# Kernel optimization log

Hardware: AMD Instinct MI355X
Metric: run time of the kernel (lower is better)

Reference implementation:

```python
import jax, jax.numpy as jnp
import numpy as np

EPS_NORM = 1e-12  # torch F.normalize eps


def _resize_bilinear_ac(x, H, W):
    # Bilinear resize with align_corners=True on NCHW tensor x.
    h, w = x.shape[-2], x.shape[-1]
    ys = jnp.linspace(0.0, h - 1.0, H)
    xs = jnp.linspace(0.0, w - 1.0, W)
    y0 = jnp.floor(ys).astype(jnp.int32); y1 = jnp.minimum(y0 + 1, h - 1)
    x0 = jnp.floor(xs).astype(jnp.int32); x1 = jnp.minimum(x0 + 1, w - 1)
    wy = (ys - y0).astype(x.dtype)[None, None, :, None]
    wx = (xs - x0).astype(x.dtype)
    rows = x[:, :, y0, :] * (1 - wy) + x[:, :, y1, :] * wy  # (B,C,H,w)
    return rows[:, :, :, x0] * (1 - wx) + rows[:, :, :, x1] * wx  # (B,C,H,W)


def _icc(p, b):
    # p: (b, 19, hw) row-stochastic over hw.
    # M[i, j] = KLDiv(input=p_i, target=p_j, batchmean) = (1/b) * sum p_j*(log p_j - p_i)
    # NOTE: original code passes probabilities (not log-probs) as KLDiv input; kept faithful.
    E = jnp.sum(p * jnp.log(p), axis=(0, 2))            # (19,) sum_b,k p log p
    G = jnp.einsum('bik,bjk->ij', p, p)                  # (19,19) sum_b,k p_i p_j
    M = (E[None, :] - G) / b
    sym = jnp.triu(M) + jnp.triu(M, 1).T                 # loop writes value for i<=j to both [i,j],[j,i]
    nrm = jnp.maximum(jnp.linalg.norm(sym, axis=1, keepdims=True), EPS_NORM)
    return sym / nrm                                     # F.normalize(dim=1)


def reference(s_out, t_out, t_logit, s_logit, conv_w, conv_b):
    T = 1.0  # temperature
    # --- pi_loss ---
    B, C, H, W = t_out.shape
    s1 = _resize_bilinear_ac(s_out, H, W)
    s1 = jnp.einsum('bchw,oc->bohw', s1, conv_w[:, :, 0, 0]) + conv_b[None, :, None, None]
    log_ps = jax.nn.log_softmax(s1 / T, axis=1)
    pt = jax.nn.softmax(t_out / T, axis=1)
    # torch KLDivLoss() default reduction='mean' (mean over ALL elements)
    pi_loss = jnp.mean(pt * (jnp.log(pt) - log_ps))
    # --- lo_loss ---
    b, n, h, w = s_logit.shape
    tl = _resize_bilinear_ac(t_logit, h, w)
    s = jax.nn.softmax(s_logit.reshape(b, n, h * w) / T, axis=2)
    t = jax.nn.softmax(tl.reshape(b, n, h * w) / T, axis=2)
    ICCS = _icc(s, b)
    ICCT = _icc(t, b)
    lo_loss = jnp.sum((ICCS - ICCT) ** 2)
    return pi_loss, lo_loss


def setup_inputs() -> dict:
    key = jax.random.key(0)
    k = jax.random.split(key, 6)
    return {
        's_out': jax.random.normal(k[0], (8, 128, 33, 33), jnp.float32),
        't_out': jax.random.normal(k[1], (8, 768, 65, 65), jnp.float32),
        't_logit': jax.random.normal(k[2], (8, 19, 65, 65), jnp.float32),
        's_logit': jax.random.normal(k[3], (8, 19, 129, 129), jnp.float32),
        'conv_w': jax.random.normal(k[4], (768, 128, 1, 1), jnp.float32) * 0.05,
        'conv_b': jax.random.normal(k[5], (768,), jnp.float32) * 0.05,
    }
```

## Files before the change

### kernel.cpp

```cpp
#include <hip/hip_runtime.h>
#include <math.h>

#define WS_E0   0
#define WS_E1   19
#define WS_G0   64
#define WS_G1   448
#define WS_Z    1152
#define WS_WBF  2048

typedef __bf16 bf16x8 __attribute__((ext_vector_type(8)));
typedef float  f32x4  __attribute__((ext_vector_type(4)));
typedef const __attribute__((address_space(1))) unsigned int guint;
typedef       __attribute__((address_space(3))) unsigned int luint;

__global__ void k_init(const float* __restrict__ conv_w, float* __restrict__ ws,
                       float* __restrict__ out) {
    const int bx = blockIdx.x, tid = threadIdx.x;
    if (bx < 96) {
        __bf16* Wb = (__bf16*)(ws + WS_WBF);
        #pragma unroll
        for (int j = 0; j < 4; j++) {
            int idx = bx * 1024 + j * 256 + tid;
            Wb[idx] = (__bf16)conv_w[idx];
        }
    } else {
        for (int k = tid; k < 2048; k += 256) ws[k] = 0.f;
        if (tid < 2) out[tid] = 0.f;
    }
}

__device__ __forceinline__ float t_resized(const float* __restrict__ Trow, int k) {
    int y = k / 129, x = k - y * 129;
    int y0 = y >> 1, x0 = x >> 1;
    int y1 = y0 + (y & 1), x1 = x0 + (x & 1);
    float fy = 0.5f * (float)(y & 1), fx = 0.5f * (float)(x & 1);
    float v00 = Trow[y0 * 65 + x0], v01 = Trow[y0 * 65 + x1];
    float v10 = Trow[y1 * 65 + x0], v11 = Trow[y1 * 65 + x1];
    float r0 = v00 + fx * (v01 - v00);
    float r1 = v10 + fx * (v11 - v10);
    return r0 + fy * (r1 - r0);
}

__launch_bounds__(256, 3)
__global__ void k_main(const float* __restrict__ s_out, const float* __restrict__ t_out,
                       const float* __restrict__ conv_w, const float* __restrict__ bias,
                       const float* __restrict__ s_logit, const float* __restrict__ t_logit,
                       float* __restrict__ ws, float* __restrict__ out) {
    __shared__ __align__(16) char lds[50176];
    const int tid = threadIdx.x;
    const int bx  = blockIdx.x;

    if (bx >= 304 && bx < 832) {
        const int idx   = bx - 304;
        const int b     = idx / 66;
        const int strip = idx - b * 66;
        const int px0   = strip * 64;

        const int l = tid & 63, g = tid >> 6, q = l >> 4, n = l & 15;
        const int og = g * 16;

        const float* base_t = t_out + (size_t)(b * 768 + og) * 4225;
        int off[4];
        #pragma unroll
        for (int j = 0; j < 4; j++) {
            int col = ((n * 4) + j * 16) & 63;
            off[j] = (j * 4 + q) * 4225 + px0 + col;
        }
        int colr[4];
        #pragma unroll
        for (int pt = 0; pt < 4; pt++)
            colr[pt] = (((pt * 16 + (n & 12) - q * 16) & 63)) + (n & 3);

        auto issue_t = [&](int cc) {
            int k = cc % 3;
            char* lb = (k == 2 ? lds : lds + 17408 + k * 16384) + g * 4096;
            const float* gb = base_t + (size_t)cc * 64 * 4225;
            #pragma unroll
            for (int j = 0; j < 4; j++)
                __builtin_amdgcn_global_load_lds((guint*)(gb + off[j]),
                                                 (luint*)(lb + j * 1024), 16, 0, 0);
        };

        issue_t(0);
        issue_t(1);

        __bf16* xs = (__bf16*)lds;

        {
            const float* Sb = s_out + b * 128 * 1089;
            #pragma unroll
            for (int ii = 0; ii < 32; ii++) {
                int id2 = tid + ii * 256;
                int c = id2 >> 6, px = id2 & 63;
                int hw = px0 + px;
                int h = hw / 65, w = hw - h * 65;
                int y0 = h >> 1, x0 = w >> 1;
                int y1 = y0 + (h & 1), x1 = x0 + (w & 1);
                float wy = 0.5f * (float)(h & 1), wx = 0.5f * (float)(w & 1);
                const float* Sc = Sb + c * 1089;
                float v00 = Sc[y0 * 33 + x0], v01 = Sc[y0 * 33 + x1];
                float v10 = Sc[y1 * 33 + x0], v11 = Sc[y1 * 33 + x1];
                float r0 = v00 + wx * (v01 - v00);
                float r1 = v10 + wx * (v11 - v10);
                xs[px * 136 + c] = (__bf16)(r0 + wy * (r1 - r0));
            }
        }
        asm volatile("s_waitcnt lgkmcnt(0)" ::: "memory");
        __builtin_amdgcn_s_barrier();
        __builtin_amdgcn_sched_barrier(0);

        bf16x8 bfrag[4][4];
        #pragma unroll
        for (int pt = 0; pt < 4; pt++)
            #pragma unroll
            for (int kf = 0; kf < 4; kf++)
                bfrag[pt][kf] = *(const bf16x8*)&xs[(pt * 16 + n) * 136 + kf * 32 + q * 8];

        const __bf16* Wbf = (const __bf16*)(ws + WS_WBF);
        bf16x8 afr[3][4];
        f32x4  bq[3];
        auto load_a = [&](int cc) {
            int s = cc % 3;
            int row0 = cc * 64 + og;
            const __bf16* Wr = Wbf + (size_t)(row0 + n) * 128 + q * 8;
            #pragma unroll
            for (int kf = 0; kf < 4; kf++) afr[s][kf] = *(const bf16x8*)(Wr + kf * 32);
            bq[s] = *(const f32x4*)&bias[row0 + q * 4];
        };
        load_a(0);
        load_a(1);

        asm volatile("s_waitcnt lgkmcnt(0)" ::: "memory");
        __builtin_amdgcn_s_barrier();
        __builtin_amdgcn_sched_barrier(0);
        issue_t(2);

        float Zt[4], St[4], Dd[4], Zs[4];
        #pragma unroll
        for (int pt = 0; pt < 4; pt++) { Zt[pt] = 0.f; St[pt] = 0.f; Dd[pt] = 0.f; Zs[pt] = 0.f; }

        #pragma unroll
        for (int c = 0; c < 12; c++) {
            if (c == 0 || c == 10) asm volatile("s_waitcnt vmcnt(9)"  ::: "memory");
            else if (c == 11)      asm volatile("s_waitcnt vmcnt(0)"  ::: "memory");
            else                   asm volatile("s_waitcnt vmcnt(13)" ::: "memory");

            const int k = c % 3;
            const float* tw = (const float*)((k == 2 ? lds : lds + 17408 + k * 16384) + g * 4096);
            #pragma unroll
            for (int pt = 0; pt < 4; pt++) {
                f32x4 a0 = {0.f, 0.f, 0.f, 0.f};
                #pragma unroll
                for (int kf = 0; kf < 4; kf++)
                    a0 = __builtin_amdgcn_mfma_f32_16x16x32_bf16(afr[k][kf], bfrag[pt][kf], a0, 0, 0, 0);
                #pragma unroll
                for (int r = 0; r < 4; r++) {
                    float tv  = tw[(q * 4 + r) * 64 + colr[pt]];
                    float s1v = a0[r] + bq[k][r];
                    float e   = __expf(tv);
                    Zt[pt] += e;
                    St[pt]  = fmaf(e, tv,  St[pt]);
                    Dd[pt]  = fmaf(e, s1v, Dd[pt]);
                    Zs[pt] += __expf(s1v);
                }
            }
            if (c <= 9) load_a(c + 2);
            if (c <= 8) issue_t(c + 3);
        }

        __syncthreads();
        float* scr = (float*)lds;
        {
            int p = g * 4 + q;
            #pragma unroll
            for (int pt = 0; pt < 4; pt++) {
                f32x4 v = {Zt[pt], St[pt], Dd[pt], Zs[pt]};
                *(f32x4*)&scr[(pt * 16 + n) * 68 + p * 4] = v;
            }
        }
        __syncthreads();
        if (tid < 64) {
            float Z = 0.f, S = 0.f, D = 0.f, Z2 = 0.f;
            #pragma unroll
            for (int p = 0; p < 16; p++) {
                f32x4 v = *(const f32x4*)&scr[tid * 68 + p * 4];
                Z += v[0]; S += v[1]; D += v[2]; Z2 += v[3];
            }
            float contrib = (S - D) / Z - logf(Z) + logf(Z2);
            #pragma unroll
            for (int o = 32; o > 0; o >>= 1) contrib += __shfl_down(contrib, o);
            if (tid == 0) atomicAdd(out, contrib * (1.0f / 25958400.0f));
        }
    } else if (bx < 304) {
        float* red = (float*)lds;
        int row  = bx;
        int side = (row >= 152) ? 1 : 0;
        int r    = side ? row - 152 : row;
        const float* src = side ? (t_logit + r * 4225) : (s_logit + r * 16641);

        float z = 0.f, s = 0.f;
        #pragma unroll 4
        for (int k = tid; k < 16641; k += 256) {
            float v = side ? t_resized(src, k) : src[k];
            float e = __expf(v);
            z += e;
            s = fmaf(e, v, s);
        }
        for (int off = 32; off > 0; off >>= 1) { z += __shfl_down(z, off); s += __shfl_down(s, off); }
        if ((tid & 63) == 0) { red[tid >> 6] = z; red[4 + (tid >> 6)] = s; }
        __syncthreads();
        if (tid == 0) {
            float Z = red[0] + red[1] + red[2] + red[3];
            float S = red[4] + red[5] + red[6] + red[7];
            ws[WS_Z + row] = Z;
            atomicAdd(&ws[(side ? WS_E1 : WS_E0) + (r % 19)], S / Z - logf(Z));
        }
    } else {
        float* xc  = (float*)lds;
        float* red = (float*)lds + 128;
        const int b = bx - 832;
        if (tid < 128) xc[tid] = s_out[((size_t)b * 128 + tid) * 1089 + 1088];
        __syncthreads();
        float z = 0.f, s = 0.f, d = 0.f, z2 = 0.f;
        #pragma unroll
        for (int rep = 0; rep < 3; rep++) {
            int o = tid + rep * 256;
            const float* Wr = conv_w + (size_t)o * 128;
            float s1 = bias[o];
            for (int cc = 0; cc < 128; cc++) s1 = fmaf(Wr[cc], xc[cc], s1);
            float tv = t_out[((size_t)(b * 768 + o)) * 4225 + 4224];
            float e  = __expf(tv);
            z += e; s = fmaf(e, tv, s); d = fmaf(e, s1, d); z2 += __expf(s1);
        }
        for (int off = 32; off > 0; off >>= 1) {
            z += __shfl_down(z, off); s += __shfl_down(s, off);
            d += __shfl_down(d, off); z2 += __shfl_down(z2, off);
        }
        if ((tid & 63) == 0) {
            int wv = tid >> 6;
            red[wv] = z; red[4 + wv] = s; red[8 + wv] = d; red[12 + wv] = z2;
        }
        __syncthreads();
        if (tid == 0) {
            float Z = red[0] + red[1] + red[2] + red[3];
            float S = red[4] + red[5] + red[6] + red[7];
            float D = red[8] + red[9] + red[10] + red[11];
            float Z2 = red[12] + red[13] + red[14] + red[15];
            float contrib = (S - D) / Z - logf(Z) + logf(Z2);
            atomicAdd(out, contrib * (1.0f / 25958400.0f));
        }
    }
}

#define KT 512
#define KP 516
__global__ void k_mid(const float* __restrict__ s_logit, const float* __restrict__ t_logit,
                      float* __restrict__ ws, float* __restrict__ out) {
    __shared__ __align__(16) char lds[39296];
    const int tid = threadIdx.x;
    const int bx  = blockIdx.x;

    float* pbuf  = (float*)lds;
    float* rowiz = (float*)(lds + 39216);
    int side = (bx >= 264) ? 1 : 0;
    int rm   = side ? bx - 264 : bx;
    int b = rm / 33, kt = rm - b * 33;
    int k0 = kt * KT;

    if (tid < 19) rowiz[tid] = 1.0f / ws[WS_Z + side * 152 + b * 19 + tid];
    __syncthreads();

    for (int i = 0; i < 19; i++) {
        const float* src = side ? (t_logit + (size_t)(b * 19 + i) * 4225)
                                : (s_logit + (size_t)(b * 19 + i) * 16641);
        float iz = rowiz[i];
        #pragma unroll
        for (int kl = tid; kl < KT; kl += 256) {
            int k = k0 + kl;
            float p = 0.f;
            if (k < 16641) {
                float v = side ? t_resized(src, k) : src[k];
                p = __expf(v) * iz;
            }
            pbuf[i * KP + kl] = p;
        }
    }
    __syncthreads();

    if (tid < 190) {
        int t = tid, i = 0;
        while (t >= 19 - i) { t -= 19 - i; i++; }
        int j = i + t;
        const float* pi_ = &pbuf[i * KP];
        const float* pj_ = &pbuf[j * KP];
        float g0 = 0.f, g1 = 0.f, g2 = 0.f, g3 = 0.f;
        #pragma unroll 2
        for (int kl = 0; kl < KT; kl += 16) {
            float4 a0 = *(const float4*)&pi_[kl];      float4 c0 = *(const float4*)&pj_[kl];
            float4 a1 = *(const float4*)&pi_[kl + 4];  float4 c1 = *(const float4*)&pj_[kl + 4];
            float4 a2 = *(const float4*)&pi_[kl + 8];  float4 c2 = *(const float4*)&pj_[kl + 8];
            float4 a3 = *(const float4*)&pi_[kl + 12]; float4 c3 = *(const float4*)&pj_[kl + 12];
            g0 = fmaf(a0.x, c0.x, g0); g0 = fmaf(a0.y, c0.y, g0);
            g0 = fmaf(a0.z, c0.z, g0); g0 = fmaf(a0.w, c0.w, g0);
            g1 = fmaf(a1.x, c1.x, g1); g1 = fmaf(a1.y, c1.y, g1);
            g1 = fmaf(a1.z, c1.z, g1); g1 = fmaf(a1.w, c1.w, g1);
            g2 = fmaf(a2.x, c2.x, g2); g2 = fmaf(a2.y, c2.y, g2);
            g2 = fmaf(a2.z, c2.z, g2); g2 = fmaf(a2.w, c2.w, g2);
            g3 = fmaf(a3.x, c3.x, g3); g3 = fmaf(a3.y, c3.y, g3);
            g3 = fmaf(a3.z, c3.z, g3); g3 = fmaf(a3.w, c3.w, g3);
        }
        atomicAdd(&ws[(side ? WS_G1 : WS_G0) + i * 19 + j], (g0 + g1) + (g2 + g3));
    }
}

__global__ void k_final(const float* __restrict__ ws, float* __restrict__ out) {
    __shared__ float Ms[361], Mt[361], ns[19], nt[19];
    __shared__ float red[8];
    int tid = threadIdx.x;
    if (tid < 361) {
        int i = tid / 19, j = tid - i * 19;
        int lo = min(i, j), hi = max(i, j);
        Ms[tid] = (ws[WS_E0 + hi] - ws[WS_G0 + lo * 19 + hi]) * 0.125f;
        Mt[tid] = (ws[WS_E1 + hi] - ws[WS_G1 + lo * 19 + hi]) * 0.125f;
    }
    __syncthreads();
    if (tid < 19) {
        float as = 0.f, at = 0.f;
        for (int j = 0; j < 19; j++) {
            as = fmaf(Ms[tid * 19 + j], Ms[tid * 19 + j], as);
            at = fmaf(Mt[tid * 19 + j], Mt[tid * 19 + j], at);
        }
        ns[tid] = fmaxf(sqrtf(as), 1e-12f);
        nt[tid] = fmaxf(sqrtf(at), 1e-12f);
    }
    __syncthreads();
    float d = 0.f;
    if (tid < 361) {
        int i = tid / 19;
        float v = Ms[tid] / ns[i] - Mt[tid] / nt[i];
        d = v * v;
    }
    for (int off = 32; off > 0; off >>= 1) d += __shfl_down(d, off);
    if ((tid & 63) == 0) red[tid >> 6] = d;
    __syncthreads();
    if (tid == 0) out[1] = red[0] + red[1] + red[2] + red[3] + red[4] + red[5];
}

extern "C" void kernel_launch(void* const* d_in, const int* in_sizes, int n_in,
                              void* d_out, int out_size, void* d_ws, size_t ws_size,
                              hipStream_t stream) {
    const float* s_out   = (const float*)d_in[0];
    const float* t_out   = (const float*)d_in[1];
    const float* t_logit = (const float*)d_in[2];
    const float* s_logit = (const float*)d_in[3];
    const float* conv_w  = (const float*)d_in[4];
    const float* conv_b  = (const float*)d_in[5];
    float* out = (float*)d_out;
    float* ws  = (float*)d_ws;

    k_init<<<dim3(97), dim3(256), 0, stream>>>(conv_w, ws, out);
    k_main<<<dim3(840), dim3(256), 0, stream>>>(s_out, t_out, conv_w, conv_b,
                                                s_logit, t_logit, ws, out);
    k_mid<<<dim3(528), dim3(256), 0, stream>>>(s_logit, t_logit, ws, out);
    k_final<<<dim3(1), dim3(384), 0, stream>>>(ws, out);
}
```

Baseline: 277.3 us.

## Reorder block roles, double-buffer weight fragments, and pin main-loop schedule

Heavy pi-loss GEMM blocks now take the lowest block indices, so they are dispatched before the lighter softmax-row blocks. The weight fragment buffer shrinks from triple to double buffering, which lowers register pressure. The main loop is manually unrolled with sched_barriers and retuned vmcnt waits so loads stay interleaved with MFMA work. The hand-counted vmcnt values depend on the exact number of outstanding loads, so a miscount could produce races or unneeded stalls.

```diff
diff --git a/kernel.cpp b/kernel.cpp
--- a/kernel.cpp
+++ b/kernel.cpp
@@ -50,10 +50,9 @@
     const int tid = threadIdx.x;
     const int bx  = blockIdx.x;
 
-    if (bx >= 304 && bx < 832) {
-        const int idx   = bx - 304;
-        const int b     = idx / 66;
-        const int strip = idx - b * 66;
+    if (bx < 528) {
+        const int b     = bx / 66;
+        const int strip = bx - b * 66;
         const int px0   = strip * 64;
 
         const int l = tid & 63, g = tid >> 6, q = l >> 4, n = l & 15;
@@ -117,10 +116,10 @@
                 bfrag[pt][kf] = *(const bf16x8*)&xs[(pt * 16 + n) * 136 + kf * 32 + q * 8];
 
         const __bf16* Wbf = (const __bf16*)(ws + WS_WBF);
-        bf16x8 afr[3][4];
-        f32x4  bq[3];
+        bf16x8 afr[2][4];
+        f32x4  bq[2];
         auto load_a = [&](int cc) {
-            int s = cc % 3;
+            int s = cc & 1;
             int row0 = cc * 64 + og;
             const __bf16* Wr = Wbf + (size_t)(row0 + n) * 128 + q * 8;
             #pragma unroll
@@ -139,34 +138,50 @@
         #pragma unroll
         for (int pt = 0; pt < 4; pt++) { Zt[pt] = 0.f; St[pt] = 0.f; Dd[pt] = 0.f; Zs[pt] = 0.f; }
 
-        #pragma unroll
-        for (int c = 0; c < 12; c++) {
-            if (c == 0 || c == 10) asm volatile("s_waitcnt vmcnt(9)"  ::: "memory");
-            else if (c == 11)      asm volatile("s_waitcnt vmcnt(0)"  ::: "memory");
-            else                   asm volatile("s_waitcnt vmcnt(13)" ::: "memory");
-
-            const int k = c % 3;
-            const float* tw = (const float*)((k == 2 ? lds : lds + 17408 + k * 16384) + g * 4096);
-            #pragma unroll
-            for (int pt = 0; pt < 4; pt++) {
-                f32x4 a0 = {0.f, 0.f, 0.f, 0.f};
-                #pragma unroll
-                for (int kf = 0; kf < 4; kf++)
-                    a0 = __builtin_amdgcn_mfma_f32_16x16x32_bf16(afr[k][kf], bfrag[pt][kf], a0, 0, 0, 0);
-                #pragma unroll
-                for (int r = 0; r < 4; r++) {
-                    float tv  = tw[(q * 4 + r) * 64 + colr[pt]];
-                    float s1v = a0[r] + bq[k][r];
-                    float e   = __expf(tv);
-                    Zt[pt] += e;
-                    St[pt]  = fmaf(e, tv,  St[pt]);
-                    Dd[pt]  = fmaf(e, s1v, Dd[pt]);
-                    Zs[pt] += __expf(s1v);
-                }
-            }
-            if (c <= 9) load_a(c + 2);
-            if (c <= 8) issue_t(c + 3);
-        }
+#define PI_IT(c, NW)                                                                     \
+        asm volatile("s_waitcnt vmcnt(" #NW ")" ::: "memory");                           \
+        __builtin_amdgcn_sched_barrier(0);                                               \
+        {                                                                                \
+            const float* tw = (const float*)((((c) % 3) == 2 ? lds                       \
+                                : lds + 17408 + ((c) % 3) * 16384) + g * 4096);          \
+            _Pragma("unroll")                                                            \
+            for (int pt = 0; pt < 4; pt++) {                                             \
+                f32x4 a0 = {0.f, 0.f, 0.f, 0.f};                                         \
+                _Pragma("unroll")                                                        \
+                for (int kf = 0; kf < 4; kf++)                                           \
+                    a0 = __builtin_amdgcn_mfma_f32_16x16x32_bf16(afr[(c) & 1][kf],       \
+                                               bfrag[pt][kf], a0, 0, 0, 0);              \
+                _Pragma("unroll")                                                        \
+                for (int r = 0; r < 4; r++) {                                            \
+                    float tv  = tw[(q * 4 + r) * 64 + colr[pt]];                         \
+                    float s1v = a0[r] + bq[(c) & 1][r];                                  \
+                    float e   = __expf(tv);                                              \
+                    Zt[pt] += e;                                                         \
+                    St[pt]  = fmaf(e, tv,  St[pt]);                                      \
+                    Dd[pt]  = fmaf(e, s1v, Dd[pt]);                                      \
+                    Zs[pt] += __expf(s1v);                                               \
+                }                                                                        \
+            }                                                                            \
+        }                                                                                \
+        __builtin_amdgcn_sched_barrier(0);                                               \
+        if ((c) <= 9) load_a((c) + 2);                                                   \
+        __builtin_amdgcn_sched_barrier(0);                                               \
+        if ((c) <= 8) issue_t((c) + 3);                                                  \
+        __builtin_amdgcn_sched_barrier(0);
+
+        PI_IT(0, 18)
+        PI_IT(1, 23)
+        PI_IT(2, 18)
+        PI_IT(3, 18)
+        PI_IT(4, 18)
+        PI_IT(5, 18)
+        PI_IT(6, 18)
+        PI_IT(7, 18)
+        PI_IT(8, 18)
+        PI_IT(9, 18)
+        PI_IT(10, 14)
+        PI_IT(11, 5)
+#undef PI_IT
 
         __syncthreads();
         float* scr = (float*)lds;
@@ -191,9 +206,9 @@
             for (int o = 32; o > 0; o >>= 1) contrib += __shfl_down(contrib, o);
             if (tid == 0) atomicAdd(out, contrib * (1.0f / 25958400.0f));
         }
-    } else if (bx < 304) {
+    } else if (bx < 832) {
         float* red = (float*)lds;
-        int row  = bx;
+        int row  = bx - 528;
         int side = (row >= 152) ? 1 : 0;
         int r    = side ? row - 152 : row;
         const float* src = side ? (t_logit + r * 4225) : (s_logit + r * 16641);
```

New measurement: 262.1 us. 1.06x faster.

## Restructure pi-loss pipeline to double buffering with per-step B-fragment LDS reads

Applied to the files above, without the earlier changes.

Switches the t_out staging from a triple buffer to a double buffer in a separate LDS region, and loads B fragments from LDS on every step instead of holding 16 bf16x8 registers. The xs stride is padded from 136 to 140 to reduce bank conflicts, and the A/bias fragments are ping-ponged through named registers via macros. The main GEMM blocks now come first in block order, ahead of the logit-row blocks, and occupancy is set with waves_per_eu. The goal is to cut register pressure so 3 waves fit, and to start the heavy blocks first. The cost is a shallower prefetch depth and more LDS reads per step.

```diff
diff --git a/kernel.cpp b/kernel.cpp
--- a/kernel.cpp
+++ b/kernel.cpp
@@ -41,19 +41,19 @@
     return r0 + fy * (r1 - r0);
 }
 
-__launch_bounds__(256, 3)
-__global__ void k_main(const float* __restrict__ s_out, const float* __restrict__ t_out,
-                       const float* __restrict__ conv_w, const float* __restrict__ bias,
-                       const float* __restrict__ s_logit, const float* __restrict__ t_logit,
-                       float* __restrict__ ws, float* __restrict__ out) {
-    __shared__ __align__(16) char lds[50176];
+__global__ __launch_bounds__(256)
+__attribute__((amdgpu_waves_per_eu(3, 3)))
+void k_main(const float* __restrict__ s_out, const float* __restrict__ t_out,
+            const float* __restrict__ conv_w, const float* __restrict__ bias,
+            const float* __restrict__ s_logit, const float* __restrict__ t_logit,
+            float* __restrict__ ws, float* __restrict__ out) {
+    __shared__ __align__(16) char lds[50688];
     const int tid = threadIdx.x;
     const int bx  = blockIdx.x;
 
-    if (bx >= 304 && bx < 832) {
-        const int idx   = bx - 304;
-        const int b     = idx / 66;
-        const int strip = idx - b * 66;
+    if (bx < 528) {
+        const int b     = bx / 66;
+        const int strip = bx - b * 66;
         const int px0   = strip * 64;
 
         const int l = tid & 63, g = tid >> 6, q = l >> 4, n = l & 15;
@@ -72,8 +72,7 @@
             colr[pt] = (((pt * 16 + (n & 12) - q * 16) & 63)) + (n & 3);
 
         auto issue_t = [&](int cc) {
-            int k = cc % 3;
-            char* lb = (k == 2 ? lds : lds + 17408 + k * 16384) + g * 4096;
+            char* lb = lds + 17920 + (cc & 1) * 16384 + g * 4096;
             const float* gb = base_t + (size_t)cc * 64 * 4225;
             #pragma unroll
             for (int j = 0; j < 4; j++)
@@ -102,71 +101,75 @@
                 float v10 = Sc[y1 * 33 + x0], v11 = Sc[y1 * 33 + x1];
                 float r0 = v00 + wx * (v01 - v00);
                 float r1 = v10 + wx * (v11 - v10);
-                xs[px * 136 + c] = (__bf16)(r0 + wy * (r1 - r0));
+                xs[px * 140 + c] = (__bf16)(r0 + wy * (r1 - r0));
             }
         }
         asm volatile("s_waitcnt lgkmcnt(0)" ::: "memory");
         __builtin_amdgcn_s_barrier();
         __builtin_amdgcn_sched_barrier(0);
 
-        bf16x8 bfrag[4][4];
-        #pragma unroll
-        for (int pt = 0; pt < 4; pt++)
-            #pragma unroll
-            for (int kf = 0; kf < 4; kf++)
-                bfrag[pt][kf] = *(const bf16x8*)&xs[(pt * 16 + n) * 136 + kf * 32 + q * 8];
-
         const __bf16* Wbf = (const __bf16*)(ws + WS_WBF);
-        bf16x8 afr[3][4];
-        f32x4  bq[3];
-        auto load_a = [&](int cc) {
-            int s = cc % 3;
-            int row0 = cc * 64 + og;
-            const __bf16* Wr = Wbf + (size_t)(row0 + n) * 128 + q * 8;
-            #pragma unroll
-            for (int kf = 0; kf < 4; kf++) afr[s][kf] = *(const bf16x8*)(Wr + kf * 32);
-            bq[s] = *(const f32x4*)&bias[row0 + q * 4];
-        };
-        load_a(0);
-        load_a(1);
-
-        asm volatile("s_waitcnt lgkmcnt(0)" ::: "memory");
-        __builtin_amdgcn_s_barrier();
-        __builtin_amdgcn_sched_barrier(0);
-        issue_t(2);
+        bf16x8 aA0, aA1, aA2, aA3, aB0, aB1, aB2, aB3;
+        f32x4  bqA, bqB;
+
+#define LOAD_A(cc, A0_, A1_, A2_, A3_, BQ_) do {                                          \
+        const __bf16* Wr_ = Wbf + (size_t)((cc) * 64 + og + n) * 128 + q * 8;             \
+        A0_ = *(const bf16x8*)(Wr_);       A1_ = *(const bf16x8*)(Wr_ + 32);              \
+        A2_ = *(const bf16x8*)(Wr_ + 64);  A3_ = *(const bf16x8*)(Wr_ + 96);              \
+        BQ_ = *(const f32x4*)&bias[(cc) * 64 + og + q * 4];                               \
+    } while (0)
+
+        LOAD_A(0, aA0, aA1, aA2, aA3, bqA);
 
         float Zt[4], St[4], Dd[4], Zs[4];
         #pragma unroll
         for (int pt = 0; pt < 4; pt++) { Zt[pt] = 0.f; St[pt] = 0.f; Dd[pt] = 0.f; Zs[pt] = 0.f; }
 
-        #pragma unroll
-        for (int c = 0; c < 12; c++) {
-            if (c == 0 || c == 10) asm volatile("s_waitcnt vmcnt(9)"  ::: "memory");
-            else if (c == 11)      asm volatile("s_waitcnt vmcnt(0)"  ::: "memory");
-            else                   asm volatile("s_waitcnt vmcnt(13)" ::: "memory");
-
-            const int k = c % 3;
-            const float* tw = (const float*)((k == 2 ? lds : lds + 17408 + k * 16384) + g * 4096);
-            #pragma unroll
-            for (int pt = 0; pt < 4; pt++) {
-                f32x4 a0 = {0.f, 0.f, 0.f, 0.f};
-                #pragma unroll
-                for (int kf = 0; kf < 4; kf++)
-                    a0 = __builtin_amdgcn_mfma_f32_16x16x32_bf16(afr[k][kf], bfrag[pt][kf], a0, 0, 0, 0);
-                #pragma unroll
-                for (int r = 0; r < 4; r++) {
-                    float tv  = tw[(q * 4 + r) * 64 + colr[pt]];
-                    float s1v = a0[r] + bq[k][r];
-                    float e   = __expf(tv);
-                    Zt[pt] += e;
-                    St[pt]  = fmaf(e, tv,  St[pt]);
-                    Dd[pt]  = fmaf(e, s1v, Dd[pt]);
-                    Zs[pt] += __expf(s1v);
-                }
-            }
-            if (c <= 9) load_a(c + 2);
-            if (c <= 8) issue_t(c + 3);
-        }
+#define PI_STEP(c, NW, A0_, A1_, A2_, A3_, BQ_, NA0_, NA1_, NA2_, NA3_, NBQ_)             \
+        asm volatile("s_waitcnt vmcnt(" #NW ")" ::: "memory");                            \
+        if ((c) < 11) LOAD_A((c) + 1, NA0_, NA1_, NA2_, NA3_, NBQ_);                      \
+        {                                                                                 \
+            const float* tw_ = (const float*)(lds + 17920 + ((c) & 1) * 16384 + g * 4096);\
+            _Pragma("unroll")                                                             \
+            for (int pt = 0; pt < 4; pt++) {                                              \
+                const __bf16* bx_ = &xs[(pt * 16 + n) * 140 + q * 8];                     \
+                bf16x8 b0_ = *(const bf16x8*)(bx_);                                       \
+                bf16x8 b1_ = *(const bf16x8*)(bx_ + 32);                                  \
+                bf16x8 b2_ = *(const bf16x8*)(bx_ + 64);                                  \
+                bf16x8 b3_ = *(const bf16x8*)(bx_ + 96);                                  \
+                f32x4 a0_ = {0.f, 0.f, 0.f, 0.f};                                         \
+                a0_ = __builtin_amdgcn_mfma_f32_16x16x32_bf16(A0_, b0_, a0_, 0, 0, 0);    \
+                a0_ = __builtin_amdgcn_mfma_f32_16x16x32_bf16(A1_, b1_, a0_, 0, 0, 0);    \
+                a0_ = __builtin_amdgcn_mfma_f32_16x16x32_bf16(A2_, b2_, a0_, 0, 0, 0);    \
+                a0_ = __builtin_amdgcn_mfma_f32_16x16x32_bf16(A3_, b3_, a0_, 0, 0, 0);    \
+                _Pragma("unroll")                                                         \
+                for (int r = 0; r < 4; r++) {                                             \
+                    float tv  = tw_[(q * 4 + r) * 64 + colr[pt]];                         \
+                    float s1v = a0_[r] + BQ_[r];                                          \
+                    float e   = __expf(tv);                                               \
+                    Zt[pt] += e;                                                          \
+                    St[pt]  = fmaf(e, tv,  St[pt]);                                       \
+                    Dd[pt]  = fmaf(e, s1v, Dd[pt]);                                       \
+                    Zs[pt] += __expf(s1v);                                                \
+                }                                                                         \
+            }                                                                             \
+        }                                                                                 \
+        if ((c) <= 9) issue_t((c) + 2);
+
+        PI_STEP(0,  4, aA0, aA1, aA2, aA3, bqA, aB0, aB1, aB2, aB3, bqB)
+        PI_STEP(1,  4, aB0, aB1, aB2, aB3, bqB, aA0, aA1, aA2, aA3, bqA)
+        PI_STEP(2,  4, aA0, aA1, aA2, aA3, bqA, aB0, aB1, aB2, aB3, bqB)
+        PI_STEP(3,  4, aB0, aB1, aB2, aB3, bqB, aA0, aA1, aA2, aA3, bqA)
+        PI_STEP(4,  4, aA0, aA1, aA2, aA3, bqA, aB0, aB1, aB2, aB3, bqB)
+        PI_STEP(5,  4, aB0, aB1, aB2, aB3, bqB, aA0, aA1, aA2, aA3, bqA)
+        PI_STEP(6,  4, aA0, aA1, aA2, aA3, bqA, aB0, aB1, aB2, aB3, bqB)
+        PI_STEP(7,  4, aB0, aB1, aB2, aB3, bqB, aA0, aA1, aA2, aA3, bqA)
+        PI_STEP(8,  4, aA0, aA1, aA2, aA3, bqA, aB0, aB1, aB2, aB3, bqB)
+        PI_STEP(9,  4, aB0, aB1, aB2, aB3, bqB, aA0, aA1, aA2, aA3, bqA)
+        PI_STEP(10, 4, aA0, aA1, aA2, aA3, bqA, aB0, aB1, aB2, aB3, bqB)
+        PI_STEP(11, 0, aB0, aB1, aB2, aB3, bqB, aA0, aA1, aA2, aA3, bqA)
+#undef PI_STEP
+#undef LOAD_A
 
         __syncthreads();
         float* scr = (float*)lds;
@@ -191,9 +194,9 @@
             for (int o = 32; o > 0; o >>= 1) contrib += __shfl_down(contrib, o);
             if (tid == 0) atomicAdd(out, contrib * (1.0f / 25958400.0f));
         }
-    } else if (bx < 304) {
+    } else if (bx < 832) {
         float* red = (float*)lds;
-        int row  = bx;
+        int row  = bx - 528;
         int side = (row >= 152) ? 1 : 0;
         int r    = side ? row - 152 : row;
         const float* src = side ? (t_logit + r * 4225) : (s_logit + r * 16641);
```

After: 243.7 us. 12.1% less time.
